# Kernel optimization log

Hardware: AMD Instinct MI355X
Metric: run time of the kernel (lower is better)

Reference implementation:

```python
import jax, jax.numpy as jnp
import numpy as np

D = 1024
B, S = 4, 2048

def setup_inputs() -> dict:
    key = jax.random.key(0)
    ks = jax.random.split(key, 9)
    scale = 1.0 / np.sqrt(D)
    return {
        "queries": jax.random.normal(ks[0], (B, S, D), dtype=jnp.float32),
        "keys": jax.random.normal(ks[1], (B, S, D), dtype=jnp.float32),
        "values": jax.random.normal(ks[2], (B, S, D), dtype=jnp.float32),
        # torch nn.Linear weights: [out, in], y = x @ W.T + b
        "Wq": jax.random.uniform(ks[3], (D, D), jnp.float32, -scale, scale),
        "bq": jax.random.uniform(ks[4], (D,), jnp.float32, -scale, scale),
        "Wk": jax.random.uniform(ks[5], (D, D), jnp.float32, -scale, scale),
        "bk": jax.random.uniform(ks[6], (D,), jnp.float32, -scale, scale),
        "Wv": jax.random.uniform(ks[7], (D, D), jnp.float32, -scale, scale),
        "bv": jax.random.uniform(ks[8], (D,), jnp.float32, -scale, scale),
    }

def reference(queries, keys, values, Wq, bq, Wk, bk, Wv, bv):
    # Linear projections (torch convention: x @ W.T + b)
    Q = jnp.einsum('bsd,ed->bse', queries, Wq) + bq  # [B,S,D]
    K = jnp.einsum('bsd,ed->bse', keys, Wk) + bk
    V = jnp.einsum('bsd,ed->bse', values, Wv) + bv
    # relu attention: no softmax, no scaling (faithful to source)
    scores = jax.nn.relu(jnp.einsum('bqd,bkd->bqk', Q, K))  # [B,S,S]
    return jnp.einsum('bqk,bkd->bqd', scores, V)
```

## Files before the change

kernel.cpp:

```cpp
#include <hip/hip_runtime.h>
#include <hip/hip_bf16.h>
#include <stdint.h>

typedef __bf16 bf16_t;
typedef __bf16 bf16x8 __attribute__((ext_vector_type(8)));
typedef float f32x16 __attribute__((ext_vector_type(16)));

#define TILE 128
#define BK 64

__device__ __forceinline__ void async_copy16(const bf16_t* g, bf16_t* l) {
    __builtin_amdgcn_global_load_lds(
        (const __attribute__((address_space(1))) unsigned int*)(uintptr_t)g,
        (__attribute__((address_space(3))) unsigned int*)(uintptr_t)l,
        16, 0, 0);
}

template<bool OUT_F32, bool RELU, int BIAS_MODE>
__global__ __launch_bounds__(256, 4)
void gemm_bt(const bf16_t* __restrict__ A, const bf16_t* __restrict__ B,
             const float* __restrict__ bias, void* __restrict__ Cp,
             int K, int ldc, long sAb, long sBb, long sCb)
{
    __shared__ bf16_t As[TILE * BK];
    __shared__ bf16_t Bs[TILE * BK];

    const int b  = blockIdx.z;
    const int nb = gridDim.x, mb = gridDim.y;
    const int SW = 4;
    int bid   = blockIdx.y * nb + blockIdx.x;
    int strip = bid / (mb * SW);
    int rem   = bid - strip * (mb * SW);
    int bm    = rem / SW;
    int bn    = strip * SW + (rem - bm * SW);
    const int blockM = bm * TILE;
    const int blockN = bn * TILE;

    const int t    = threadIdx.x;
    const int lane = t & 63;
    const int wave = t >> 6;
    const int wm   = (wave >> 1) * 64;
    const int wn   = (wave & 1) * 64;
    const int r32  = lane & 31;
    const int half = lane >> 5;
    const int kx   = r32 & 7;

    f32x16 acc[2][2] = {};

    const bf16_t* Ab = A + sAb * (long)b;
    const bf16_t* Bb = B + sBb * (long)b;

    const bf16_t* gA[4]; const bf16_t* gB[4];
    bf16_t* lA[4]; bf16_t* lB[4];
    #pragma unroll
    for (int j = 0; j < 4; j++) {
        int c   = t + j * 256;
        int row = c >> 3;
        int kcl = (c & 7) ^ (row & 7);
        gA[j] = Ab + (long)(blockM + row) * K + kcl * 8;
        gB[j] = Bb + (long)(blockN + row) * K + kcl * 8;
        lA[j] = &As[c * 8];
        lB[j] = &Bs[c * 8];
    }

    for (int k0 = 0; k0 < K; k0 += BK) {
        #pragma unroll
        for (int j = 0; j < 4; j++) async_copy16(gA[j] + k0, lA[j]);
        #pragma unroll
        for (int j = 0; j < 4; j++) async_copy16(gB[j] + k0, lB[j]);
        __syncthreads();

        #pragma unroll
        for (int ks = 0; ks < 4; ks++) {
            const int kc = ks * 2 + half;
            bf16x8 af[2], bfr[2];
            #pragma unroll
            for (int i = 0; i < 2; i++) {
                int R = wm + i * 32 + r32;
                af[i] = *(const bf16x8*)&As[(R * 8 + (kc ^ kx)) * 8];
            }
            #pragma unroll
            for (int j = 0; j < 2; j++) {
                int C = wn + j * 32 + r32;
                bfr[j] = *(const bf16x8*)&Bs[(C * 8 + (kc ^ kx)) * 8];
            }
            #pragma unroll
            for (int i = 0; i < 2; i++)
                #pragma unroll
                for (int j = 0; j < 2; j++)
                    acc[i][j] = __builtin_amdgcn_mfma_f32_32x32x16_bf16(
                                    af[i], bfr[j], acc[i][j], 0, 0, 0);
        }
        __syncthreads();
    }

    float*  Cf = (float*) Cp + sCb * (long)b;
    bf16_t* Ch = (bf16_t*)Cp + sCb * (long)b;
    #pragma unroll
    for (int ti = 0; ti < 2; ti++) {
        #pragma unroll
        for (int tj = 0; tj < 2; tj++) {
            const int gcol = blockN + wn + tj * 32 + r32;
            float bc = 0.f;
            if (BIAS_MODE == 1) bc = bias[gcol];
            #pragma unroll
            for (int reg = 0; reg < 16; reg++) {
                const int grow = blockM + wm + ti * 32
                               + (reg & 3) + 8 * (reg >> 2) + 4 * half;
                float vv = acc[ti][tj][reg];
                if (BIAS_MODE == 1) vv += bc;
                if (BIAS_MODE == 2) vv += bias[grow];
                if (RELU) vv = fmaxf(vv, 0.f);
                if (OUT_F32) Cf[(long)grow * ldc + gcol] = vv;
                else         Ch[(long)grow * ldc + gcol] = (bf16_t)vv;
            }
        }
    }
}

__global__ __launch_bounds__(256)
void cast_all_kernel(const float* __restrict__ q, const float* __restrict__ k,
                     const float* __restrict__ v, const float* __restrict__ Wq,
                     const float* __restrict__ Wk, const float* __restrict__ Wv,
                     bf16_t* __restrict__ ws)
{
    const long BIG = 1048576;
    const long SMALL = 131072;
    long id = (long)blockIdx.x * blockDim.x + threadIdx.x;
    const float* src; bf16_t* dst;
    if (id < 3 * BIG) {
        int s = (int)(id / BIG);
        long off = (id - (long)s * BIG) * 8;
        src = (s == 0 ? q : s == 1 ? k : v) + off;
        dst = ws + (long)s * 8388608 + off;
    } else {
        long id2 = id - 3 * BIG;
        int s = (int)(id2 / SMALL);
        long off = (id2 - (long)s * SMALL) * 8;
        src = (s == 0 ? Wq : s == 1 ? Wk : Wv) + off;
        dst = ws + 25165824L + (long)s * 1048576 + off;
    }
    float4 v0 = ((const float4*)src)[0];
    float4 v1 = ((const float4*)src)[1];
    alignas(16) bf16_t o[8];
    o[0]=(bf16_t)v0.x; o[1]=(bf16_t)v0.y; o[2]=(bf16_t)v0.z; o[3]=(bf16_t)v0.w;
    o[4]=(bf16_t)v1.x; o[5]=(bf16_t)v1.y; o[6]=(bf16_t)v1.z; o[7]=(bf16_t)v1.w;
    *(uint4*)dst = *(const uint4*)o;
}

extern "C" void kernel_launch(void* const* d_in, const int* in_sizes, int n_in,
                              void* d_out, int out_size, void* d_ws, size_t ws_size,
                              hipStream_t stream)
{
    const float* q   = (const float*)d_in[0];
    const float* k   = (const float*)d_in[1];
    const float* v   = (const float*)d_in[2];
    const float* Wq  = (const float*)d_in[3];
    const float* bq  = (const float*)d_in[4];
    const float* Wk  = (const float*)d_in[5];
    const float* bk  = (const float*)d_in[6];
    const float* Wv  = (const float*)d_in[7];
    const float* bv  = (const float*)d_in[8];

    const int B = 4, S = 2048, D = 1024;
    const int BS = B * S;

    bf16_t* ws  = (bf16_t*)d_ws;
    bf16_t* qb  = ws;
    bf16_t* kb  = ws + 8388608L;
    bf16_t* vb  = ws + 16777216L;
    bf16_t* Wqb = ws + 25165824L;
    bf16_t* Wkb = ws + 26214400L;
    bf16_t* Wvb = ws + 27262976L;
    bf16_t* Qp  = ws + 28311552L;
    bf16_t* Kp  = ws + 36700160L;
    bf16_t* VpT = ws + 45088768L;
    bf16_t* Sc  = ws;

    dim3 blk(256);

    cast_all_kernel<<<dim3(13824), blk, 0, stream>>>(q, k, v, Wq, Wk, Wv, ws);

    gemm_bt<false, false, 1><<<dim3(D / TILE, BS / TILE, 1), blk, 0, stream>>>(
        qb, Wqb, bq, Qp, D, D, 0L, 0L, 0L);

    gemm_bt<false, false, 1><<<dim3(D / TILE, BS / TILE, 1), blk, 0, stream>>>(
        kb, Wkb, bk, Kp, D, D, 0L, 0L, 0L);

    gemm_bt<false, false, 2><<<dim3(S / TILE, D / TILE, B), blk, 0, stream>>>(
        Wvb, vb, bv, VpT, D, S, 0L, (long)S * D, (long)D * S);

    gemm_bt<false, true, 0><<<dim3(S / TILE, S / TILE, B), blk, 0, stream>>>(
        Qp, Kp, nullptr, Sc, D, S, (long)S * D, (long)S * D, (long)S * S);

    gemm_bt<true, false, 0><<<dim3(D / TILE, S / TILE, B), blk, 0, stream>>>(
        Sc, VpT, nullptr, d_out, S, D, (long)S * S, (long)D * S, (long)S * D);
}
```

Baseline: 316.4 us.

## Replace GEMM with 256x256 double-buffered ping-pong MFMA kernel

Replaces the 128x128 single-buffered GEMM with a 256x256-tile kernel using 512 threads and a 128KB double-buffered LDS. Global-to-LDS copies of the next K tile are interleaved with 16x16x32 MFMA phases, with explicit vmcnt waits, barriers and s_setprio, so memory transfer overlaps compute. Blocks are also remapped across XCDs in strides of eight. The larger tiles raise data reuse and cut sync stalls. The cost is fewer blocks per GEMM (128 for most launches), which may leave CUs idle, and only one block fits per CU because of the LDS size.

```diff
diff --git a/kernel.cpp b/kernel.cpp
--- a/kernel.cpp
+++ b/kernel.cpp
@@ -4,10 +4,7 @@
 
 typedef __bf16 bf16_t;
 typedef __bf16 bf16x8 __attribute__((ext_vector_type(8)));
-typedef float f32x16 __attribute__((ext_vector_type(16)));
-
-#define TILE 128
-#define BK 64
+typedef float  f32x4  __attribute__((ext_vector_type(4)));
 
 __device__ __forceinline__ void async_copy16(const bf16_t* g, bf16_t* l) {
     __builtin_amdgcn_global_load_lds(
@@ -16,104 +13,173 @@
         16, 0, 0);
 }
 
+#define BARR()  asm volatile("s_barrier" ::: "memory")
+#define VMW(n)  asm volatile("s_waitcnt vmcnt(" #n ")" ::: "memory")
+
+
+#define STAGEA(buf, h, kt) do {                                                   \
+    _Pragma("unroll") for (int j = 0; j < 2; j++)                                 \
+        async_copy16(ApM + (long)(h)*128*K + (long)(kt)*64 + offJ[j],             \
+                     (bf16_t*)(lds + (buf)*65536 + (h)*16384 + ldst_[j]));        \
+} while (0)
+
+#define STAGEB(buf, h, kt) do {                                                   \
+    _Pragma("unroll") for (int j = 0; j < 2; j++)                                 \
+        async_copy16(BpN + (long)(h)*128*K + (long)(kt)*64 + offJ[j],             \
+                     (bf16_t*)(lds + (buf)*65536 + 32768 + (h)*16384 + ldst_[j]));\
+} while (0)
+
+#define LOADA(buf, hA) do {                                                       \
+    _Pragma("unroll") for (int m = 0; m < 4; m++)                                 \
+    _Pragma("unroll") for (int ks = 0; ks < 2; ks++) {                            \
+        const int R = (hA)*128 + sr*64 + m*16 + l15;                              \
+        afr[m][ks] = *(const bf16x8*)(lds + (buf)*65536 + R*128                   \
+                                      + (((ks*4 + l4) ^ (l15 & 7)) << 4));        \
+    } } while (0)
+
+#define LOADB(buf, hB) do {                                                       \
+    _Pragma("unroll") for (int n = 0; n < 2; n++)                                 \
+    _Pragma("unroll") for (int ks = 0; ks < 2; ks++) {                            \
+        const int Cc = (hB)*128 + sc*32 + n*16 + l15;                             \
+        bfr[hB][n][ks] = *(const bf16x8*)(lds + (buf)*65536 + 32768 + Cc*128      \
+                                          + (((ks*4 + l4) ^ (l15 & 7)) << 4));    \
+    } } while (0)
+
+#define MMA(hA, hB) do {                                                          \
+    __builtin_amdgcn_s_setprio(1);                                                \
+    _Pragma("unroll") for (int m = 0; m < 4; m++)                                 \
+    _Pragma("unroll") for (int n = 0; n < 2; n++)                                 \
+    _Pragma("unroll") for (int ks = 0; ks < 2; ks++)                              \
+        acc[hA][hB][m][n] = __builtin_amdgcn_mfma_f32_16x16x32_bf16(              \
+            afr[m][ks], bfr[hB][n][ks], acc[hA][hB][m][n], 0, 0, 0);              \
+    __builtin_amdgcn_s_setprio(0);                                                \
+} while (0)
+
 template<bool OUT_F32, bool RELU, int BIAS_MODE>
-__global__ __launch_bounds__(256, 4)
-void gemm_bt(const bf16_t* __restrict__ A, const bf16_t* __restrict__ B,
+__global__ __launch_bounds__(512, 2)
+void gemm256(const bf16_t* __restrict__ A, const bf16_t* __restrict__ B,
              const float* __restrict__ bias, void* __restrict__ Cp,
              int K, int ldc, long sAb, long sBb, long sCb)
 {
-    __shared__ bf16_t As[TILE * BK];
-    __shared__ bf16_t Bs[TILE * BK];
-
-    const int b  = blockIdx.z;
-    const int nb = gridDim.x, mb = gridDim.y;
-    const int SW = 4;
-    int bid   = blockIdx.y * nb + blockIdx.x;
-    int strip = bid / (mb * SW);
-    int rem   = bid - strip * (mb * SW);
-    int bm    = rem / SW;
-    int bn    = strip * SW + (rem - bm * SW);
-    const int blockM = bm * TILE;
-    const int blockN = bn * TILE;
+    __shared__ char lds[131072];
+
+    const int gx = gridDim.x, gy = gridDim.y;
+    const int tot = gx * gy * gridDim.z;
+    const int lin = (blockIdx.z * gy + blockIdx.y) * gx + blockIdx.x;
+    const int q8  = tot >> 3;
+    const int wg  = (lin & 7) * q8 + (lin >> 3);
+    const int bz  = wg / (gx * gy);
+    const int r2  = wg - bz * gx * gy;
+    const int by  = r2 / gx;
+    const int bx  = r2 - by * gx;
+    const int blockM = by * 256;
+    const int blockN = bx * 256;
 
     const int t    = threadIdx.x;
     const int lane = t & 63;
     const int wave = t >> 6;
-    const int wm   = (wave >> 1) * 64;
-    const int wn   = (wave & 1) * 64;
-    const int r32  = lane & 31;
-    const int half = lane >> 5;
-    const int kx   = r32 & 7;
-
-    f32x16 acc[2][2] = {};
-
-    const bf16_t* Ab = A + sAb * (long)b;
-    const bf16_t* Bb = B + sBb * (long)b;
-
-    const bf16_t* gA[4]; const bf16_t* gB[4];
-    bf16_t* lA[4]; bf16_t* lB[4];
-    #pragma unroll
-    for (int j = 0; j < 4; j++) {
-        int c   = t + j * 256;
-        int row = c >> 3;
-        int kcl = (c & 7) ^ (row & 7);
-        gA[j] = Ab + (long)(blockM + row) * K + kcl * 8;
-        gB[j] = Bb + (long)(blockN + row) * K + kcl * 8;
-        lA[j] = &As[c * 8];
-        lB[j] = &Bs[c * 8];
-    }
-
-    for (int k0 = 0; k0 < K; k0 += BK) {
+    const int sr   = wave >> 2;
+    const int sc   = wave & 3;
+    const int l15  = lane & 15;
+    const int l4   = lane >> 4;
+
+    const bf16_t* Ab  = A + sAb * (long)bz;
+    const bf16_t* Bb  = B + sBb * (long)bz;
+    const bf16_t* ApM = Ab + (long)blockM * K;
+    const bf16_t* BpN = Bb + (long)blockN * K;
+
+    long     offJ[2];
+    uint32_t ldst_[2];
+    #pragma unroll
+    for (int j = 0; j < 2; j++) {
+        const int c = t + j * 512;
+        const int r = c >> 3, s = c & 7;
+        offJ[j]  = (long)r * K + ((s ^ (r & 7)) * 8);
+        ldst_[j] = (uint32_t)c * 16;
+    }
+
+    f32x4  acc[2][2][4][2] = {};
+    bf16x8 afr[4][2];
+    bf16x8 bfr[2][2][2];
+
+    const int NT = K >> 6;
+    const int NI = NT >> 1;
+
+    STAGEA(0, 0, 0); STAGEB(0, 0, 0); STAGEA(0, 1, 0); STAGEB(0, 1, 0);
+    STAGEA(1, 0, 1); STAGEB(1, 0, 1);
+    VMW(4);
+    BARR();
+
+    for (int i = 0; i < NI; ++i) {
+        const int  T    = 2 * i;
+        const bool last = (i == NI - 1);
+
+        LOADA(0, 0); LOADB(0, 0);
+        STAGEA(1, 1, T + 1);
+        BARR();
+        MMA(0, 0);
+        VMW(6);
+        BARR();
+        LOADB(0, 1);
+        STAGEB(1, 1, T + 1);
+        BARR();
+        MMA(0, 1);
+        BARR();
+        LOADA(0, 1);
+        if (!last) STAGEA(0, 0, T + 2);
+        BARR();
+        MMA(1, 0);
+        BARR();
+        if (!last) STAGEB(0, 0, T + 2);
+        BARR();
+        MMA(1, 1);
+        if (last) { VMW(0); } else { VMW(6); }
+        BARR();
+        LOADA(1, 0); LOADB(1, 0);
+        if (!last) STAGEA(0, 1, T + 2);
+        BARR();
+        MMA(0, 0);
+        if (!last) VMW(6);
+        BARR();
+        LOADB(1, 1);
+        if (!last) STAGEB(0, 1, T + 2);
+        BARR();
+        MMA(0, 1);
+        BARR();
+        LOADA(1, 1);
+        if (!last) STAGEA(1, 0, T + 3);
+        BARR();
+        MMA(1, 0);
+        BARR();
+        if (!last) STAGEB(1, 0, T + 3);
+        BARR();
+        MMA(1, 1);
+        if (!last) VMW(6);
+        BARR();
+    }
+
+    float*  Cf = (float*) Cp + sCb * (long)bz;
+    bf16_t* Ch = (bf16_t*)Cp + sCb * (long)bz;
+    #pragma unroll
+    for (int hA = 0; hA < 2; hA++)
+    #pragma unroll
+    for (int hB = 0; hB < 2; hB++)
+    #pragma unroll
+    for (int m = 0; m < 4; m++)
+    #pragma unroll
+    for (int n = 0; n < 2; n++) {
+        const int gcol = blockN + hB * 128 + sc * 32 + n * 16 + l15;
+        float bc = 0.f;
+        if (BIAS_MODE == 1) bc = bias[gcol];
         #pragma unroll
-        for (int j = 0; j < 4; j++) async_copy16(gA[j] + k0, lA[j]);
-        #pragma unroll
-        for (int j = 0; j < 4; j++) async_copy16(gB[j] + k0, lB[j]);
-        __syncthreads();
-
-        #pragma unroll
-        for (int ks = 0; ks < 4; ks++) {
-            const int kc = ks * 2 + half;
-            bf16x8 af[2], bfr[2];
-            #pragma unroll
-            for (int i = 0; i < 2; i++) {
-                int R = wm + i * 32 + r32;
-                af[i] = *(const bf16x8*)&As[(R * 8 + (kc ^ kx)) * 8];
-            }
-            #pragma unroll
-            for (int j = 0; j < 2; j++) {
-                int C = wn + j * 32 + r32;
-                bfr[j] = *(const bf16x8*)&Bs[(C * 8 + (kc ^ kx)) * 8];
-            }
-            #pragma unroll
-            for (int i = 0; i < 2; i++)
-                #pragma unroll
-                for (int j = 0; j < 2; j++)
-                    acc[i][j] = __builtin_amdgcn_mfma_f32_32x32x16_bf16(
-                                    af[i], bfr[j], acc[i][j], 0, 0, 0);
-        }
-        __syncthreads();
-    }
-
-    float*  Cf = (float*) Cp + sCb * (long)b;
-    bf16_t* Ch = (bf16_t*)Cp + sCb * (long)b;
-    #pragma unroll
-    for (int ti = 0; ti < 2; ti++) {
-        #pragma unroll
-        for (int tj = 0; tj < 2; tj++) {
-            const int gcol = blockN + wn + tj * 32 + r32;
-            float bc = 0.f;
-            if (BIAS_MODE == 1) bc = bias[gcol];
-            #pragma unroll
-            for (int reg = 0; reg < 16; reg++) {
-                const int grow = blockM + wm + ti * 32
-                               + (reg & 3) + 8 * (reg >> 2) + 4 * half;
-                float vv = acc[ti][tj][reg];
-                if (BIAS_MODE == 1) vv += bc;
-                if (BIAS_MODE == 2) vv += bias[grow];
-                if (RELU) vv = fmaxf(vv, 0.f);
-                if (OUT_F32) Cf[(long)grow * ldc + gcol] = vv;
-                else         Ch[(long)grow * ldc + gcol] = (bf16_t)vv;
-            }
+        for (int reg = 0; reg < 4; reg++) {
+            const int grow = blockM + hA * 128 + sr * 64 + m * 16 + l4 * 4 + reg;
+            float vv = acc[hA][hB][m][n][reg];
+            if (BIAS_MODE == 1) vv += bc;
+            if (BIAS_MODE == 2) vv += bias[grow];
+            if (RELU) vv = fmaxf(vv, 0.f);
+            if (OUT_F32) Cf[(long)grow * ldc + gcol] = vv;
+            else         Ch[(long)grow * ldc + gcol] = (bf16_t)vv;
         }
     }
 }
@@ -163,7 +229,6 @@
     const float* bv  = (const float*)d_in[8];
 
     const int B = 4, S = 2048, D = 1024;
-    const int BS = B * S;
 
     bf16_t* ws  = (bf16_t*)d_ws;
     bf16_t* qb  = ws;
@@ -177,22 +242,22 @@
     bf16_t* VpT = ws + 45088768L;
     bf16_t* Sc  = ws;
 
-    dim3 blk(256);
-
-    cast_all_kernel<<<dim3(13824), blk, 0, stream>>>(q, k, v, Wq, Wk, Wv, ws);
-
-    gemm_bt<false, false, 1><<<dim3(D / TILE, BS / TILE, 1), blk, 0, stream>>>(
+    cast_all_kernel<<<dim3(13824), dim3(256), 0, stream>>>(q, k, v, Wq, Wk, Wv, ws);
+
+    dim3 blk(512);
+
+    gemm256<false, false, 1><<<dim3(4, 32, 1), blk, 0, stream>>>(
         qb, Wqb, bq, Qp, D, D, 0L, 0L, 0L);
 
-    gemm_bt<false, false, 1><<<dim3(D / TILE, BS / TILE, 1), blk, 0, stream>>>(
+    gemm256<false, false, 1><<<dim3(4, 32, 1), blk, 0, stream>>>(
         kb, Wkb, bk, Kp, D, D, 0L, 0L, 0L);
 
-    gemm_bt<false, false, 2><<<dim3(S / TILE, D / TILE, B), blk, 0, stream>>>(
+    gemm256<false, false, 2><<<dim3(8, 4, 4), blk, 0, stream>>>(
         Wvb, vb, bv, VpT, D, S, 0L, (long)S * D, (long)D * S);
 
-    gemm_bt<false, true, 0><<<dim3(S / TILE, S / TILE, B), blk, 0, stream>>>(
+    gemm256<false, true, 0><<<dim3(8, 8, 4), blk, 0, stream>>>(
         Qp, Kp, nullptr, Sc, D, S, (long)S * D, (long)S * D, (long)S * S);
 
-    gemm_bt<true, false, 0><<<dim3(D / TILE, S / TILE, B), blk, 0, stream>>>(
+    gemm256<true, false, 0><<<dim3(4, 8, 4), blk, 0, stream>>>(
         Sc, VpT, nullptr, d_out, S, D, (long)S * S, (long)D * S, (long)S * D);
 }
```

Result: slower. 326.5 us (+3.2%).
